# Optimization experiments

Hardware: AMD Instinct MI355X
Metric: run time of the kernel (lower is better)

Reference implementation:

```python
import jax, jax.numpy as jnp
import numpy as np

B, S, D = 8, 1024, 1024
H, DK, DV = 16, 64, 64
OUT = 64  # out_size; W_o output dim = OUT * H = 1024


def setup_inputs() -> dict:
    key = jax.random.key(0)
    ks = jax.random.split(key, 8)
    queries = jax.random.normal(ks[0], (B, S, D), dtype=jnp.float32)
    keys = jax.random.normal(ks[1], (B, S, D), dtype=jnp.float32)
    values = jax.random.normal(ks[2], (B, S, D), dtype=jnp.float32)
    # Linear weights stored as [in, out] (no bias per bias=False)
    Wq = jax.random.normal(ks[3], (D, DK * H), dtype=jnp.float32) * 0.02
    Wk = jax.random.normal(ks[4], (D, DK * H), dtype=jnp.float32) * 0.02
    Wv = jax.random.normal(ks[5], (D, DV * H), dtype=jnp.float32) * 0.02
    Wo = jax.random.normal(ks[6], (DV * H, OUT * H), dtype=jnp.float32) * 0.02
    valid_lens = jax.random.randint(ks[7], (B,), 1, S + 1, dtype=jnp.int32)
    return {"queries": queries, "keys": keys, "values": values,
            "Wq": Wq, "Wk": Wk, "Wv": Wv, "Wo": Wo, "valid_lens": valid_lens}


def reference(queries, keys, values, Wq, Wk, Wv, Wo, valid_lens):
    b, s, _ = queries.shape
    # projections + transpose_qkv: [B,S,H*dh] -> [B,H,S,dh]
    q = (queries @ Wq).reshape(b, s, H, DK).transpose(0, 2, 1, 3)
    k = (keys @ Wk).reshape(b, keys.shape[1], H, DK).transpose(0, 2, 1, 3)
    v = (values @ Wv).reshape(b, values.shape[1], H, DV).transpose(0, 2, 1, 3)
    scale = DK ** 0.5  # epsilon = 0.0
    scores = jnp.einsum('bhqd,bhkd->bhqk', q, k) / scale
    # valid_lens masking on last axis: masked entries set to -1e6 (not -inf)
    kv_len = k.shape[2]
    mask = jnp.arange(kv_len)[None, None, None, :] < valid_lens[:, None, None, None]
    scores = jnp.where(mask, scores, -1e6)
    attn = jax.nn.softmax(scores, axis=-1)  # dropout p=0.0 -> identity
    out = jnp.einsum('bhqk,bhkd->bhqd', attn, v)
    # transpose_output: [B,H,S,dv] -> [B,S,H*dv]
    out = out.transpose(0, 2, 1, 3).reshape(b, s, H * DV)
    return out @ Wo
```

## Files before the change

### kernel.cpp

```cpp
#include <hip/hip_runtime.h>
#include <hip/hip_bf16.h>
#include <stdint.h>

typedef __bf16 bf16_t;
typedef __bf16 bf16x8 __attribute__((ext_vector_type(8)));
typedef float f32x4 __attribute__((ext_vector_type(4)));

#define B_  8
#define S_  1024
#define D_  1024
#define H_  16
#define DH_ 64

static __device__ __forceinline__ f32x4 mfma_bf16(bf16x8 a, bf16x8 b, f32x4 c) {
  return __builtin_amdgcn_mfma_f32_16x16x32_bf16(a, b, c, 0, 0, 0);
}

#define GLOAD_LDS16(g, l)                                                     \
  __builtin_amdgcn_global_load_lds(                                           \
      (const __attribute__((address_space(1))) void*)(g),                     \
      (__attribute__((address_space(3))) void*)(l), 16, 0, 0)

__global__ __launch_bounds__(256) void transpose4(
    const float* __restrict__ w0, const float* __restrict__ w1,
    const float* __restrict__ w2, const float* __restrict__ w3,
    bf16_t* __restrict__ t0, bf16_t* __restrict__ t1,
    bf16_t* __restrict__ t2, bf16_t* __restrict__ t3)
{
  __shared__ float tile[64][65];
  const float* src; bf16_t* dst;
  switch (blockIdx.z) {
    case 0: src = w0; dst = t0; break;
    case 1: src = w1; dst = t1; break;
    case 2: src = w2; dst = t2; break;
    default: src = w3; dst = t3; break;
  }
  const int tx = threadIdx.x & 63;
  const int ty = threadIdx.x >> 6;
  const int c0 = blockIdx.x * 64, r0 = blockIdx.y * 64;
#pragma unroll
  for (int r = ty; r < 64; r += 4)
    tile[r][tx] = src[(size_t)(r0 + r) * 1024 + c0 + tx];
  __syncthreads();
#pragma unroll
  for (int r = ty; r < 64; r += 4)
    dst[(size_t)(c0 + r) * 1024 + r0 + tx] = (bf16_t)tile[tx][r];
}

__global__ __launch_bounds__(256) void convert_qkv(
    const float* __restrict__ q, const float* __restrict__ k,
    const float* __restrict__ v,
    bf16_t* __restrict__ qo, bf16_t* __restrict__ ko, bf16_t* __restrict__ vo)
{
  const float* src; bf16_t* dst;
  switch (blockIdx.y) {
    case 0: src = q; dst = qo; break;
    case 1: src = k; dst = ko; break;
    default: src = v; dst = vo; break;
  }
  const size_t i = ((size_t)blockIdx.x * 256 + threadIdx.x) * 8;
  float4 a = *(const float4*)(src + i);
  float4 b = *(const float4*)(src + i + 4);
  bf16x8 o;
  o[0] = (bf16_t)a.x; o[1] = (bf16_t)a.y; o[2] = (bf16_t)a.z; o[3] = (bf16_t)a.w;
  o[4] = (bf16_t)b.x; o[5] = (bf16_t)b.y; o[6] = (bf16_t)b.z; o[7] = (bf16_t)b.w;
  *(bf16x8*)(dst + i) = o;
}

__global__ __launch_bounds__(256) void transposeV(
    const bf16_t* __restrict__ src, bf16_t* __restrict__ dst)
{
  __shared__ bf16_t t[64 * 72];
  const size_t base = (size_t)blockIdx.y * (64 * 1024);
  const int s0 = blockIdx.x * 64;
#pragma unroll
  for (int it = 0; it < 2; ++it) {
    const int c = it * 256 + threadIdx.x;
    const int r = c >> 3, col8 = (c & 7) * 8;
    bf16x8 v = *(const bf16x8*)(src + base + (size_t)(s0 + r) * 64 + col8);
    *(bf16x8*)(t + r * 72 + col8) = v;
  }
  __syncthreads();
#pragma unroll
  for (int it = 0; it < 2; ++it) {
    const int c = it * 256 + threadIdx.x;
    const int d = c >> 3, sc8 = (c & 7) * 8;
    bf16x8 v;
#pragma unroll
    for (int j = 0; j < 8; ++j) v[j] = t[(sc8 + j) * 72 + d];
    *(bf16x8*)(dst + base + (size_t)d * 1024 + s0 + sc8) = v;
  }
}

#define BM_G 256
#define BN_G 128
#define BK_G 64
#define KDIM 1024
#define NK_G (KDIM / BK_G)
#define ATILE (BM_G * BK_G)
#define BTILE (BN_G * BK_G)
#define LDS_BYTES ((3 * (ATILE + BTILE)) * 2)

template <int MODE>
__device__ __forceinline__ void gemm_core(
    const bf16_t* __restrict__ Ap, const bf16_t* __restrict__ Bp,
    void* __restrict__ Cp, bf16_t* smem)
{
  bf16_t* const As = smem;
  bf16_t* const Bs = smem + 3 * ATILE;

  const int tid  = threadIdx.x;
  const int wv   = tid >> 6;
  const int lane = tid & 63;
  const int wm   = wv >> 1;
  const int wn   = wv & 1;
  const int quad = lane >> 4;
  const int l15  = lane & 15;

  const int xcd   = blockIdx.x & 7;
  const int rblk  = blockIdx.x >> 3;
  const int tileM = xcd * 4 + (rblk & 3);
  const int tileN = rblk >> 2;

  const int lr  = lane >> 3;
  const int swz = (((lane & 7) ^ lr) << 3);
  const bf16_t* gA0 = Ap + (size_t)(tileM * BM_G + wv * 8 + lr) * KDIM + swz;
  const bf16_t* gB0 = Bp + (size_t)(tileN * BN_G + wv * 8 + lr) * KDIM + swz;
  const int lA0 = wv * 8 * BK_G;
  const int lB0 = wv * 8 * BK_G;

#define STAGE_TILE(koff, bA, bB) do {                                          \
    GLOAD_LDS16(gA0 + (koff),                       As + (bA) + lA0);          \
    GLOAD_LDS16(gA0 + (size_t)64  * KDIM + (koff),  As + (bA) + lA0 + 64*BK_G); \
    GLOAD_LDS16(gA0 + (size_t)128 * KDIM + (koff),  As + (bA) + lA0 + 128*BK_G);\
    GLOAD_LDS16(gA0 + (size_t)192 * KDIM + (koff),  As + (bA) + lA0 + 192*BK_G);\
    GLOAD_LDS16(gB0 + (koff),                       Bs + (bB) + lB0);          \
    GLOAD_LDS16(gB0 + (size_t)64  * KDIM + (koff),  Bs + (bB) + lB0 + 64*BK_G); \
  } while (0)

  f32x4 acc[4][4];
#pragma unroll
  for (int mi = 0; mi < 4; ++mi)
#pragma unroll
    for (int ni = 0; ni < 4; ++ni)
      acc[mi][ni] = (f32x4){0.f, 0.f, 0.f, 0.f};

  STAGE_TILE(0, 0, 0);
  STAGE_TILE(BK_G, ATILE, BTILE);

  int cbA = 0, cbB = 0;
  int sbA = 2 * ATILE, sbB = 2 * BTILE;

  for (int t = 0; t < NK_G; ++t) {
    if (t + 2 < NK_G) STAGE_TILE((size_t)(t + 2) * BK_G, sbA, sbB);

    if (t < NK_G - 2)       asm volatile("s_waitcnt vmcnt(12)" ::: "memory");
    else if (t == NK_G - 2) asm volatile("s_waitcnt vmcnt(6)" ::: "memory");
    else                    asm volatile("s_waitcnt vmcnt(0)" ::: "memory");
    __builtin_amdgcn_s_barrier();
    asm volatile("" ::: "memory");

    bf16x8 af[2][4], bfr[2][4];
#pragma unroll
    for (int kk = 0; kk < 2; ++kk) {
      const int sl = (((quad + (kk << 2)) ^ (l15 & 7)) << 3);
#pragma unroll
      for (int mi = 0; mi < 4; ++mi)
        af[kk][mi] = *(const bf16x8*)(As + cbA + (wm * 64 + mi * 16 + l15) * BK_G + sl);
#pragma unroll
      for (int ni = 0; ni < 4; ++ni)
        bfr[kk][ni] = *(const bf16x8*)(Bs + cbB + (wn * 64 + ni * 16 + l15) * BK_G + sl);
    }
    __builtin_amdgcn_s_setprio(1);
#pragma unroll
    for (int kk = 0; kk < 2; ++kk)
#pragma unroll
      for (int mi = 0; mi < 4; ++mi)
#pragma unroll
        for (int ni = 0; ni < 4; ++ni)
          acc[mi][ni] = mfma_bf16(af[kk][mi], bfr[kk][ni], acc[mi][ni]);
    __builtin_amdgcn_s_setprio(0);

    asm volatile("" ::: "memory");
    __builtin_amdgcn_s_barrier();

    cbA += ATILE; if (cbA == 3 * ATILE) cbA = 0;
    cbB += BTILE; if (cbB == 3 * BTILE) cbB = 0;
    sbA += ATILE; if (sbA == 3 * ATILE) sbA = 0;
    sbB += BTILE; if (sbB == 3 * BTILE) sbB = 0;
  }
#undef STAGE_TILE

#pragma unroll
  for (int mi = 0; mi < 4; ++mi) {
#pragma unroll
    for (int ni = 0; ni < 4; ++ni) {
#pragma unroll
      for (int r = 0; r < 4; ++r) {
        const int row = tileM * BM_G + wm * 64 + mi * 16 + quad * 4 + r;
        const int col = tileN * BN_G + wn * 64 + ni * 16 + l15;
        if (MODE == 0) {
          ((float*)Cp)[(size_t)row * 1024 + col] = acc[mi][ni][r];
        } else {
          const int b = row >> 10, s = row & 1023;
          const int h = col >> 6,  d = col & 63;
          ((bf16_t*)Cp)[(((size_t)(b * H_ + h) << 10) | s) * DH_ + d] =
              (bf16_t)acc[mi][ni][r];
        }
      }
    }
  }
}

__global__ __launch_bounds__(512, 2) void gemm_proj(
    const bf16_t* __restrict__ A0, const bf16_t* __restrict__ A1, const bf16_t* __restrict__ A2,
    const bf16_t* __restrict__ B0, const bf16_t* __restrict__ B1, const bf16_t* __restrict__ B2,
    bf16_t* __restrict__ C0, bf16_t* __restrict__ C1, bf16_t* __restrict__ C2)
{
  extern __shared__ bf16_t smem[];
  const bf16_t* Ap; const bf16_t* Bp; bf16_t* Cp;
  if (blockIdx.z == 0)      { Ap = A0; Bp = B0; Cp = C0; }
  else if (blockIdx.z == 1) { Ap = A1; Bp = B1; Cp = C1; }
  else                      { Ap = A2; Bp = B2; Cp = C2; }
  gemm_core<1>(Ap, Bp, (void*)Cp, smem);
}

__global__ __launch_bounds__(512, 2) void gemm_out(
    const bf16_t* __restrict__ Ap, const bf16_t* __restrict__ Bp,
    float* __restrict__ Cp)
{
  extern __shared__ bf16_t smem[];
  gemm_core<0>(Ap, Bp, (void*)Cp, smem);
}

__global__ __launch_bounds__(256) void attn64(
    const bf16_t* __restrict__ Q,
    const bf16_t* __restrict__ Kv,
    const bf16_t* __restrict__ Vt,
    const int* __restrict__ valid_lens,
    bf16_t* __restrict__ O)
{
  const int h  = blockIdx.x;
  const int qt = blockIdx.y;
  const int b  = blockIdx.z;
  const int tid  = threadIdx.x;
  const int wave = tid >> 6;
  const int lane = tid & 63;
  const int quad = lane >> 4;
  const int l15  = lane & 15;

  const int L   = valid_lens[b];
  const int nkt = (L + 63) >> 6;

  const size_t base = ((size_t)(b * H_ + h)) * S_ * DH_;
  const bf16_t* Qp = Q  + base;
  const bf16_t* Kp = Kv + base;
  const bf16_t* Vp = Vt + base;

  __shared__ bf16_t KsA[64 * 32];
  __shared__ bf16_t KsB[64 * 32];
  __shared__ bf16_t VsA[64 * 32];
  __shared__ bf16_t VsB[64 * 32];
  __shared__ bf16_t Pb[4][16 * 72];
  bf16_t* const Pw = &Pb[wave][0];

  const int sr = tid >> 2;
  const int sj = (tid & 3) << 3;
  const int ldsOff = (wave * 64) * 8;

  const int qrow = qt * 64 + wave * 16 + l15;
  const bf16x8 qf0 = *(const bf16x8*)(Qp + (size_t)qrow * DH_ + quad * 8);
  const bf16x8 qf1 = *(const bf16x8*)(Qp + (size_t)qrow * DH_ + 32 + quad * 8);

  f32x4 o[4];
  float lsum[4];
#pragma unroll
  for (int r = 0; r < 4; ++r) {
    o[r] = (f32x4){0.f, 0.f, 0.f, 0.f};
    lsum[r] = 0.f;
  }

  for (int kt = 0; kt < nkt; ++kt) {
    const int k0 = kt * 64;

    __syncthreads();
    GLOAD_LDS16(Kp + (size_t)(k0 + sr) * DH_ + sj,      KsA + ldsOff);
    GLOAD_LDS16(Kp + (size_t)(k0 + sr) * DH_ + 32 + sj, KsB + ldsOff);
    GLOAD_LDS16(Vp + (size_t)sr * S_ + k0 + sj,         VsA + ldsOff);
    GLOAD_LDS16(Vp + (size_t)sr * S_ + k0 + 32 + sj,    VsB + ldsOff);
    __syncthreads();

    f32x4 sc[4];
#pragma unroll
    for (int n16 = 0; n16 < 4; ++n16) {
      const int row = (n16 * 16 + l15) * 32 + quad * 8;
      bf16x8 kf0 = *(const bf16x8*)(KsA + row);
      bf16x8 kf1 = *(const bf16x8*)(KsB + row);
      f32x4 s = (f32x4){0.f, 0.f, 0.f, 0.f};
      s = mfma_bf16(qf0, kf0, s);
      s = mfma_bf16(qf1, kf1, s);
      sc[n16] = s;
    }

    if (k0 + 64 <= L) {
#pragma unroll
      for (int n16 = 0; n16 < 4; ++n16) {
#pragma unroll
        for (int r = 0; r < 4; ++r) {
          const float p = __expf(sc[n16][r] * 0.125f);
          lsum[r] += p;
          Pw[(quad * 4 + r) * 72 + n16 * 16 + l15] = (bf16_t)p;
        }
      }
    } else {
#pragma unroll
      for (int n16 = 0; n16 < 4; ++n16) {
        const bool valid = (k0 + n16 * 16 + l15) < L;
#pragma unroll
        for (int r = 0; r < 4; ++r) {
          const float p = valid ? __expf(sc[n16][r] * 0.125f) : 0.f;
          lsum[r] += p;
          Pw[(quad * 4 + r) * 72 + n16 * 16 + l15] = (bf16_t)p;
        }
      }
    }

    const bf16x8 pf0 = *(const bf16x8*)(Pw + l15 * 72 + quad * 8);
    const bf16x8 pf1 = *(const bf16x8*)(Pw + l15 * 72 + 32 + quad * 8);
#pragma unroll
    for (int dt = 0; dt < 4; ++dt) {
      const int row = (dt * 16 + l15) * 32 + quad * 8;
      bf16x8 vf0 = *(const bf16x8*)(VsA + row);
      bf16x8 vf1 = *(const bf16x8*)(VsB + row);
      o[dt] = mfma_bf16(pf0, vf0, o[dt]);
      o[dt] = mfma_bf16(pf1, vf1, o[dt]);
    }
  }

  float inv[4];
#pragma unroll
  for (int r = 0; r < 4; ++r) {
    float t = lsum[r];
    t += __shfl_xor(t, 1, 64);
    t += __shfl_xor(t, 2, 64);
    t += __shfl_xor(t, 4, 64);
    t += __shfl_xor(t, 8, 64);
    inv[r] = 1.f / t;
  }
  const int qout = qt * 64 + wave * 16 + quad * 4;
#pragma unroll
  for (int dt = 0; dt < 4; ++dt) {
#pragma unroll
    for (int r = 0; r < 4; ++r) {
      const float v = o[dt][r] * inv[r];
      O[((size_t)(b * S_ + qout + r)) * (H_ * DH_) + h * DH_ + dt * 16 + l15] = (bf16_t)v;
    }
  }
}

extern "C" void kernel_launch(void* const* d_in, const int* in_sizes, int n_in,
                              void* d_out, int out_size, void* d_ws, size_t ws_size,
                              hipStream_t stream) {
  const float* queries = (const float*)d_in[0];
  const float* keys    = (const float*)d_in[1];
  const float* values  = (const float*)d_in[2];
  const float* Wq      = (const float*)d_in[3];
  const float* Wk      = (const float*)d_in[4];
  const float* Wv      = (const float*)d_in[5];
  const float* Wo      = (const float*)d_in[6];
  const int* valid_lens = (const int*)d_in[7];
  float* out = (float*)d_out;

  bf16_t* ws = (bf16_t*)d_ws;
  const size_t MB = 1024 * 1024;
  bf16_t* WqT = ws + 0 * MB;
  bf16_t* WkT = ws + 1 * MB;
  bf16_t* WvT = ws + 2 * MB;
  bf16_t* WoT = ws + 3 * MB;
  bf16_t* Qc  = ws + 4 * MB;
  bf16_t* Kc  = ws + 12 * MB;
  bf16_t* Vc  = ws + 20 * MB;
  bf16_t* Qb  = ws + 28 * MB;
  bf16_t* Kb  = ws + 36 * MB;
  bf16_t* Vb  = ws + 44 * MB;
  bf16_t* VbT = ws + 52 * MB;
  bf16_t* Ab  = ws + 60 * MB;

  (void)hipFuncSetAttribute((const void*)gemm_proj,
                            hipFuncAttributeMaxDynamicSharedMemorySize, LDS_BYTES);
  (void)hipFuncSetAttribute((const void*)gemm_out,
                            hipFuncAttributeMaxDynamicSharedMemorySize, LDS_BYTES);

  transpose4<<<dim3(16, 16, 4), 256, 0, stream>>>(Wq, Wk, Wv, Wo, WqT, WkT, WvT, WoT);

  convert_qkv<<<dim3(4096, 3), 256, 0, stream>>>(queries, keys, values, Qc, Kc, Vc);

  gemm_proj<<<dim3(256, 1, 3), 512, LDS_BYTES, stream>>>(Qc, Kc, Vc,
                                                         WqT, WkT, WvT,
                                                         Qb, Kb, Vb);

  transposeV<<<dim3(16, 128), 256, 0, stream>>>(Vb, VbT);

  attn64<<<dim3(16, 16, 8), 256, 0, stream>>>(Qb, Kb, VbT, valid_lens, Ab);

  gemm_out<<<dim3(256, 1, 1), 512, LDS_BYTES, stream>>>(Ab, WoT, out);
}
```

Before: 295.6 us.

## Split GEMM main loop into two phases interleaving prefetch with MFMA

Restructures the projection GEMM's K loop into two half-phases. Each phase loads half of the A fragments, issues half of the next tile's global-to-LDS prefetches, then runs the MFMAs for those rows, with explicit barriers and sched_barriers between phases. The aim is to spread memory issue across the compute so LDS reads, global loads and MFMAs overlap better, in a ping-pong style schedule. The cost is extra barriers per iteration and tighter wait-count bookkeeping, which may stall the waves.

```diff
diff --git a/kernel.cpp b/kernel.cpp
--- a/kernel.cpp
+++ b/kernel.cpp
@@ -129,6 +129,13 @@
   const int lA0 = wv * 8 * BK_G;
   const int lB0 = wv * 8 * BK_G;
 
+  f32x4 acc[4][4];
+#pragma unroll
+  for (int mi = 0; mi < 4; ++mi)
+#pragma unroll
+    for (int ni = 0; ni < 4; ++ni)
+      acc[mi][ni] = (f32x4){0.f, 0.f, 0.f, 0.f};
+
 #define STAGE_TILE(koff, bA, bB) do {                                          \
     GLOAD_LDS16(gA0 + (koff),                       As + (bA) + lA0);          \
     GLOAD_LDS16(gA0 + (size_t)64  * KDIM + (koff),  As + (bA) + lA0 + 64*BK_G); \
@@ -138,49 +145,80 @@
     GLOAD_LDS16(gB0 + (size_t)64  * KDIM + (koff),  Bs + (bB) + lB0 + 64*BK_G); \
   } while (0)
 
-  f32x4 acc[4][4];
-#pragma unroll
-  for (int mi = 0; mi < 4; ++mi)
-#pragma unroll
-    for (int ni = 0; ni < 4; ++ni)
-      acc[mi][ni] = (f32x4){0.f, 0.f, 0.f, 0.f};
-
   STAGE_TILE(0, 0, 0);
   STAGE_TILE(BK_G, ATILE, BTILE);
+  asm volatile("s_waitcnt vmcnt(6)" ::: "memory");
+  __builtin_amdgcn_s_barrier();
 
   int cbA = 0, cbB = 0;
   int sbA = 2 * ATILE, sbB = 2 * BTILE;
 
   for (int t = 0; t < NK_G; ++t) {
-    if (t + 2 < NK_G) STAGE_TILE((size_t)(t + 2) * BK_G, sbA, sbB);
-
-    if (t < NK_G - 2)       asm volatile("s_waitcnt vmcnt(12)" ::: "memory");
-    else if (t == NK_G - 2) asm volatile("s_waitcnt vmcnt(6)" ::: "memory");
-    else                    asm volatile("s_waitcnt vmcnt(0)" ::: "memory");
-    __builtin_amdgcn_s_barrier();
-    asm volatile("" ::: "memory");
-
-    bf16x8 af[2][4], bfr[2][4];
+    const bool havePf = (t + 2 < NK_G);
+    const size_t koff = (size_t)(t + 2) * BK_G;
+
+    bf16x8 afA[2][2], bfr[2][4];
 #pragma unroll
     for (int kk = 0; kk < 2; ++kk) {
       const int sl = (((quad + (kk << 2)) ^ (l15 & 7)) << 3);
 #pragma unroll
-      for (int mi = 0; mi < 4; ++mi)
-        af[kk][mi] = *(const bf16x8*)(As + cbA + (wm * 64 + mi * 16 + l15) * BK_G + sl);
+      for (int mi = 0; mi < 2; ++mi)
+        afA[kk][mi] = *(const bf16x8*)(As + cbA + (wm * 64 + mi * 16 + l15) * BK_G + sl);
 #pragma unroll
       for (int ni = 0; ni < 4; ++ni)
         bfr[kk][ni] = *(const bf16x8*)(Bs + cbB + (wn * 64 + ni * 16 + l15) * BK_G + sl);
     }
+    if (havePf) {
+      GLOAD_LDS16(gA0 + koff,                       As + sbA + lA0);
+      GLOAD_LDS16(gA0 + (size_t)64  * KDIM + koff,  As + sbA + lA0 + 64 * BK_G);
+      GLOAD_LDS16(gA0 + (size_t)128 * KDIM + koff,  As + sbA + lA0 + 128 * BK_G);
+    }
+    asm volatile("" ::: "memory");
+    __builtin_amdgcn_s_barrier();
+    asm volatile("s_waitcnt lgkmcnt(0)" ::: "memory");
+    __builtin_amdgcn_sched_barrier(0);
     __builtin_amdgcn_s_setprio(1);
 #pragma unroll
     for (int kk = 0; kk < 2; ++kk)
 #pragma unroll
-      for (int mi = 0; mi < 4; ++mi)
+      for (int mi = 0; mi < 2; ++mi)
 #pragma unroll
         for (int ni = 0; ni < 4; ++ni)
-          acc[mi][ni] = mfma_bf16(af[kk][mi], bfr[kk][ni], acc[mi][ni]);
+          acc[mi][ni] = mfma_bf16(afA[kk][mi], bfr[kk][ni], acc[mi][ni]);
     __builtin_amdgcn_s_setprio(0);
-
+    __builtin_amdgcn_sched_barrier(0);
+    asm volatile("" ::: "memory");
+    __builtin_amdgcn_s_barrier();
+
+    bf16x8 afB[2][2];
+#pragma unroll
+    for (int kk = 0; kk < 2; ++kk) {
+      const int sl = (((quad + (kk << 2)) ^ (l15 & 7)) << 3);
+#pragma unroll
+      for (int mi = 0; mi < 2; ++mi)
+        afB[kk][mi] = *(const bf16x8*)(As + cbA + (wm * 64 + (mi + 2) * 16 + l15) * BK_G + sl);
+    }
+    if (havePf) {
+      GLOAD_LDS16(gA0 + (size_t)192 * KDIM + koff,  As + sbA + lA0 + 192 * BK_G);
+      GLOAD_LDS16(gB0 + koff,                       Bs + sbB + lB0);
+      GLOAD_LDS16(gB0 + (size_t)64  * KDIM + koff,  Bs + sbB + lB0 + 64 * BK_G);
+    }
+    asm volatile("" ::: "memory");
+    __builtin_amdgcn_s_barrier();
+    asm volatile("s_waitcnt lgkmcnt(0)" ::: "memory");
+    __builtin_amdgcn_sched_barrier(0);
+    __builtin_amdgcn_s_setprio(1);
+#pragma unroll
+    for (int kk = 0; kk < 2; ++kk)
+#pragma unroll
+      for (int mi = 0; mi < 2; ++mi)
+#pragma unroll
+        for (int ni = 0; ni < 4; ++ni)
+          acc[mi + 2][ni] = mfma_bf16(afB[kk][mi], bfr[kk][ni], acc[mi + 2][ni]);
+    __builtin_amdgcn_s_setprio(0);
+    __builtin_amdgcn_sched_barrier(0);
+    if (havePf)             asm volatile("s_waitcnt vmcnt(6)" ::: "memory");
+    else if (t + 1 < NK_G)  asm volatile("s_waitcnt vmcnt(0)" ::: "memory");
     asm volatile("" ::: "memory");
     __builtin_amdgcn_s_barrier();
 
```

New measurement: 288.8 us. 2.3% less time.
